# Kernel tuning notes

Measured on AMD Instinct MI355X. Metric: run time of the kernel, lower is better.

Reference implementation:

```python
import jax, jax.numpy as jnp
import numpy as np
from jax import lax
from jax.scipy.linalg import solve_triangular

T, DX, DZ = 8192, 1024, 16
POS_CONST = 1e-6
THRESH = 1e-5


def setup_inputs() -> dict:
    key = jax.random.key(0)
    ks = jax.random.split(key, 7)
    s = 0.02  # small init scale so A ~ I and AA is well-conditioned for Cholesky
    return {
        "X": jax.random.normal(ks[0], (T, DX), jnp.float32),
        "W1": jax.random.normal(ks[1], (DX, DX), jnp.float32) * s,
        "b1": jnp.zeros((DX,), jnp.float32),
        "Wmu": jax.random.normal(ks[2], (DX, DZ), jnp.float32) * s,
        "bmu": jnp.zeros((DZ,), jnp.float32),
        "WA": jax.random.normal(ks[3], (DX, DZ * DZ), jnp.float32) * s,
        "bA": jnp.zeros((DZ * DZ,), jnp.float32),
        "WB": jax.random.normal(ks[4], (2 * DX, DZ * DZ), jnp.float32) * s,
        "bB": jnp.zeros((DZ * DZ,), jnp.float32),
        "eps": jax.random.normal(ks[5], (T, DZ), jnp.float32),
    }


def _blk_tridag_chol(AA, BB):
    # AA: (T, d, d) diagonal blocks, BB: (T-1, d, d) lower off-diagonal blocks.
    # Returns lower-bidiagonal block Cholesky: chol_A (T,d,d), chol_B (T-1,d,d).
    L0 = jnp.linalg.cholesky(AA[0])

    def step(Lprev, ins):
        Bt, At = ins
        # C = Bt @ inv(Lprev)^T, via triangular solve: Lprev C^T = Bt^T
        C = solve_triangular(Lprev, Bt.T, lower=True).T
        Lt = jnp.linalg.cholesky(At - C @ C.T)
        return Lt, (Lt, C)

    _, (Ls, Cs) = lax.scan(step, L0, (BB, AA[1:]))
    return jnp.concatenate([L0[None], Ls]), Cs


def _blk_chol_inv_identity(chol_A, chol_B):
    # Forward substitution L x = b with b = block-diagonal identity blocks.
    I = jnp.eye(DZ, dtype=chol_A.dtype)
    x0 = solve_triangular(chol_A[0], I, lower=True)

    def step(xprev, ins):
        Lt, Ct = ins
        xt = solve_triangular(Lt, I - Ct @ xprev, lower=True)
        return xt, xt

    _, xs = lax.scan(step, x0, (chol_A[1:], chol_B))
    return jnp.concatenate([x0[None], xs])


def reference(X, W1, b1, Wmu, bmu, WA, bA, WB, bB, eps):
    # encode
    h = jax.nn.relu(X @ W1 + b1)                       # (T, dx)
    mu = h @ Wmu + bmu                                 # (T, dz)
    A = (h @ WA + bA).reshape(T, DZ, DZ) + jnp.eye(DZ, dtype=X.dtype)
    hcat = jnp.concatenate([h[1:], h[:-1]], axis=1)    # (T-1, 2*dx)
    B = (hcat @ WB + bB).reshape(T - 1, DZ, DZ)

    # make_psd
    diag_sq = jnp.einsum('tij,tkj->tik', A, A)         # A A^T
    offd_sq = jnp.einsum('tij,tkj->tik', B, B)         # B B^T
    offd_sq = jnp.concatenate([jnp.zeros((1, DZ, DZ), X.dtype), offd_sq])
    AA = diag_sq + offd_sq + POS_CONST * jnp.eye(DZ, dtype=X.dtype)
    BB = jnp.einsum('tij,tkj->tik', B, A[:-1])         # B A[:-1]^T

    chol_A, chol_B = _blk_tridag_chol(AA, BB)
    r = _blk_chol_inv_identity(chol_A, chol_B)         # (T, dz, dz)

    # relu(r - thresh) + thresh == max(r, thresh)
    r = jax.nn.relu(r - THRESH) + THRESH
    logdet = -jnp.log(jnp.einsum('tii->ti', r)).sum()
    entropy = logdet + DX * T / 2.0 * (1.0 + np.log(2.0 * np.pi))

    # sample_z = mu + r^T eps per block
    sample_z = mu + jnp.einsum('tji,tj->ti', r, eps)
    return entropy, sample_z
```

## Files before the change

### kernel.cpp

```cpp
#include <hip/hip_runtime.h>
#include <math.h>


#define T_STEPS 8192
#define DXX 1024

typedef __bf16 bf16x8 __attribute__((ext_vector_type(8)));
typedef float f32x4 __attribute__((ext_vector_type(4)));
typedef unsigned short u16x8 __attribute__((ext_vector_type(8)));
typedef unsigned short u16x4 __attribute__((ext_vector_type(4)));

typedef __attribute__((address_space(1))) unsigned int as1_uint;
typedef __attribute__((address_space(3))) unsigned int as3_uint;

#define DOT4(r, b) ((r).x*(b).x + (r).y*(b).y + (r).z*(b).z + (r).w*(b).w)

__device__ __forceinline__ unsigned short f2bf(float v) {
  unsigned int u = __float_as_uint(v);
  unsigned int r = (u + 0x7FFFu + ((u >> 16) & 1u)) >> 16;
  return (unsigned short)r;
}
__device__ __forceinline__ float bf2f(unsigned short b) {
  return __uint_as_float(((unsigned int)b) << 16);
}

__device__ __forceinline__ void gload16(const unsigned short* g, unsigned short* s) {
  __builtin_amdgcn_global_load_lds((as1_uint*)g, (as3_uint*)s, 16, 0, 0);
}

__global__ __launch_bounds__(256) void to_bf16(
    const float* __restrict__ src, unsigned short* __restrict__ dst, int n4)
{
  int idx = blockIdx.x * 256 + threadIdx.x;
  if (idx >= n4) return;
  float4 v = ((const float4*)src)[idx];
  u16x4 h;
  h[0] = f2bf(v.x); h[1] = f2bf(v.y); h[2] = f2bf(v.z); h[3] = f2bf(v.w);
  *(u16x4*)(dst + (size_t)idx * 4) = h;
}

__global__ __launch_bounds__(256) void transpose_bf16(
    const float* __restrict__ W, unsigned short* __restrict__ Tt, int K, int N)
{
  __shared__ float tile[32][33];
  int k0 = blockIdx.x * 32, n0 = blockIdx.y * 32;
  int c = threadIdx.x & 31, r = threadIdx.x >> 5;
#pragma unroll
  for (int e = 0; e < 4; ++e)
    tile[r + 8 * e][c] = W[(size_t)(k0 + r + 8 * e) * N + n0 + c];
  __syncthreads();
#pragma unroll
  for (int e = 0; e < 4; ++e)
    Tt[(size_t)(n0 + r + 8 * e) * K + k0 + c] = f2bf(tile[c][r + 8 * e]);
}

#define GBK 64

__global__ __launch_bounds__(256) void gemm_mfma(
    const unsigned short* __restrict__ Abf, const unsigned short* __restrict__ Bbf,
    const float* __restrict__ bias, int biasN, float* __restrict__ outF,
    unsigned short* __restrict__ outBf, int M, int N, int K, int mode)
{
  __shared__ __align__(16) unsigned short At[128 * GBK];
  __shared__ __align__(16) unsigned short Bt[128 * GBK];
  int tid = threadIdx.x;
  int l = tid & 63;
  int w = tid >> 6;
  int wm = w >> 1, wn = w & 1;
  int lane15 = l & 15, quad = l >> 4;
  int bm = blockIdx.y * 128, bn = blockIdx.x * 128;

  int srow = (w << 3) + (l >> 3);
  int jswz = (l & 7) ^ (srow & 7);
  const unsigned short* aSrc = Abf + (size_t)(bm + srow) * K + jswz * 8;
  const unsigned short* bSrc = Bbf + (size_t)(bn + srow) * K + jswz * 8;

  f32x4 acc[4][4];
#pragma unroll
  for (int mi = 0; mi < 4; ++mi)
#pragma unroll
    for (int ni = 0; ni < 4; ++ni) acc[mi][ni] = (f32x4){0.f, 0.f, 0.f, 0.f};

  for (int k0 = 0; k0 < K; k0 += GBK) {
#pragma unroll
    for (int i = 0; i < 4; ++i) {
      gload16(aSrc + (size_t)(i * 32) * K + k0, &At[(i * 32 + (w << 3)) * GBK]);
      gload16(bSrc + (size_t)(i * 32) * K + k0, &Bt[(i * 32 + (w << 3)) * GBK]);
    }
    __syncthreads();
#pragma unroll
    for (int h = 0; h < 2; ++h) {
      bf16x8 af[4], bfr[4];
#pragma unroll
      for (int mi = 0; mi < 4; ++mi) {
        int r = wm * 64 + mi * 16 + lane15;
        af[mi] = *(const bf16x8*)&At[r * GBK + ((((h << 2) + quad) ^ (lane15 & 7)) << 3)];
      }
#pragma unroll
      for (int ni = 0; ni < 4; ++ni) {
        int r = wn * 64 + ni * 16 + lane15;
        bfr[ni] = *(const bf16x8*)&Bt[r * GBK + ((((h << 2) + quad) ^ (lane15 & 7)) << 3)];
      }
#pragma unroll
      for (int mi = 0; mi < 4; ++mi)
#pragma unroll
        for (int ni = 0; ni < 4; ++ni)
          acc[mi][ni] = __builtin_amdgcn_mfma_f32_16x16x32_bf16(af[mi], bfr[ni], acc[mi][ni], 0, 0, 0);
    }
    __syncthreads();
  }

#pragma unroll
  for (int mi = 0; mi < 4; ++mi) {
#pragma unroll
    for (int ni = 0; ni < 4; ++ni) {
      int gc = bn + wn * 64 + ni * 16 + lane15;
      float bv = (bias && gc < biasN) ? bias[gc] : 0.f;
#pragma unroll
      for (int r = 0; r < 4; ++r) {
        int gr = bm + wm * 64 + mi * 16 + quad * 4 + r;
        float v = acc[mi][ni][r] + bv;
        if (mode == 1) {
          outBf[(size_t)gr * N + gc] = f2bf(fmaxf(v, 0.f));
        } else {
          outF[(size_t)gr * N + gc] = v;
        }
      }
    }
  }
}

__global__ __launch_bounds__(256) void mu_gemm(
    const unsigned short* __restrict__ hbf, const float* __restrict__ Wmu,
    const float* __restrict__ bmu, float* __restrict__ mu)
{
  int idx = blockIdx.x * 256 + threadIdx.x;
  int t = idx >> 4, j = idx & 15;
  const u16x8* ph = (const u16x8*)(hbf + (size_t)t * 1024);
  float s = bmu[j];
#pragma unroll 2
  for (int k8 = 0; k8 < 128; ++k8) {
    u16x8 hv = ph[k8];
#pragma unroll
    for (int e = 0; e < 8; ++e)
      s = fmaf(bf2f(hv[e]), Wmu[(k8 * 8 + e) * 16 + j], s);
  }
  mu[idx] = s;
}

__global__ __launch_bounds__(256) void make_psd(
    const float* __restrict__ Ccat, const float* __restrict__ bB,
    float* __restrict__ AAT, float* __restrict__ BBm, float* __restrict__ logdet)
{
  int t = blockIdx.x;
  int tid = threadIdx.x;
  int i = tid >> 4, j = tid & 15;
  if (t == 0 && tid == 0) *logdet = 0.f;
  __shared__ float a[16][17], bp[16][17], bq[16][17];
  a[i][j] = Ccat[(size_t)t * 768 + tid] + (i == j ? 1.f : 0.f);
  bp[i][j] = (t >= 1) ? (Ccat[(size_t)t * 768 + 256 + tid] + Ccat[(size_t)(t - 1) * 768 + 512 + tid] + bB[tid]) : 0.f;
  bool has_b = (t < T_STEPS - 1);
  if (has_b) bq[i][j] = Ccat[(size_t)(t + 1) * 768 + 256 + tid] + Ccat[(size_t)t * 768 + 512 + tid] + bB[tid];
  __syncthreads();
  float s = (i == j) ? 1e-6f : 0.f;
#pragma unroll
  for (int k = 0; k < 16; ++k) s += a[i][k] * a[j][k] + bp[i][k] * bp[j][k];
  AAT[(size_t)t * 256 + ((i >> 2) * 64 + j * 4 + (i & 3))] = s;
  if (has_b) {
    float s2 = 0.f;
#pragma unroll
    for (int k = 0; k < 16; ++k) s2 += bq[i][k] * a[j][k];
    BBm[(size_t)t * 256 + tid] = s2;
  }
}

#define RIC_S 8
#define RIC_W 16
#define RIC_NCH (T_STEPS / RIC_S)

__global__ __launch_bounds__(64) void riccati_wave(
    const float* __restrict__ AAT, const float* __restrict__ BBm,
    float* __restrict__ D)
{
  int l = threadIdx.x;
  int q = l >> 4, c = l & 15;
  int p = blockIdx.x;
  int t0 = p * RIC_S;
  int tw = t0 - RIC_W; if (tw < 0) tw = 0;
  int tend = t0 + RIC_S - 1;
  int row = l >> 2, cb = (l & 3) * 4;

  __shared__ float bbs[320], dis[320], ys[320];

  float4 a4 = *(const float4*)(AAT + (size_t)tw * 256 + l * 4);
  float dr[4] = {a4.x, a4.y, a4.z, a4.w};

  for (int t = tw; ; ++t) {
    if (t >= t0) {
#pragma unroll
      for (int u = 0; u < 4; ++u)
        D[(size_t)t * 256 + (q * 4 + u) * 16 + c] = dr[u];
    }
    if (t == tend) break;
    float4 bb4 = *(const float4*)(BBm + (size_t)t * 256 + l * 4);
    float4 aar = *(const float4*)(AAT + (size_t)(t + 1) * 256 + l * 4);

#pragma unroll
    for (int k = 0; k < 16; ++k) {
      const int kq = k >> 2, ku = k & 3;
      float rowv = __shfl(dr[ku], (kq << 4) | c);
      float pv   = __uint_as_float(__builtin_amdgcn_readlane(__float_as_uint(dr[ku]), (kq << 4) | k));
      float cv0  = __shfl(dr[0], (l & 48) | k);
      float cv1  = __shfl(dr[1], (l & 48) | k);
      float cv2  = __shfl(dr[2], (l & 48) | k);
      float cv3  = __shfl(dr[3], (l & 48) | k);
      float rpv  = __builtin_amdgcn_rcpf(pv);
      float t1v  = rowv * rpv;
      float cva[4] = {cv0, cv1, cv2, cv3};
#pragma unroll
      for (int u = 0; u < 4; ++u) {
        bool irow = (q == kq) && (u == ku);
        float nv = irow ? ((c == k) ? rpv : t1v)
                        : ((c == k) ? (-cva[u] * rpv) : fmaf(-cva[u], t1v, dr[u]));
        dr[u] = nv;
      }
    }

    *(float4*)&bbs[row * 20 + cb] = bb4;
#pragma unroll
    for (int u = 0; u < 4; ++u) dis[(q * 4 + u) * 20 + c] = dr[u];

    float y0a = 0, y1a = 0, y2a = 0, y3a = 0;
    float y0b = 0, y1b = 0, y2b = 0, y3b = 0;
#pragma unroll
    for (int kb = 0; kb < 4; ++kb) {
      float4 bc4 = *(const float4*)&bbs[c * 20 + kb * 4];
      float4 r0 = *(const float4*)&dis[(q * 4 + 0) * 20 + kb * 4];
      float4 r1 = *(const float4*)&dis[(q * 4 + 1) * 20 + kb * 4];
      float4 r2 = *(const float4*)&dis[(q * 4 + 2) * 20 + kb * 4];
      float4 r3 = *(const float4*)&dis[(q * 4 + 3) * 20 + kb * 4];
      if (kb & 1) {
        y0b += DOT4(r0, bc4); y1b += DOT4(r1, bc4); y2b += DOT4(r2, bc4); y3b += DOT4(r3, bc4);
      } else {
        y0a += DOT4(r0, bc4); y1a += DOT4(r1, bc4); y2a += DOT4(r2, bc4); y3a += DOT4(r3, bc4);
      }
    }
    ys[(q * 4 + 0) * 20 + c] = y0a + y0b;
    ys[(q * 4 + 1) * 20 + c] = y1a + y1b;
    ys[(q * 4 + 2) * 20 + c] = y2a + y2b;
    ys[(q * 4 + 3) * 20 + c] = y3a + y3b;

    float s0a = aar.x, s1a = aar.y, s2a = aar.z, s3a = aar.w;
    float s0b = 0, s1b = 0, s2b = 0, s3b = 0;
#pragma unroll
    for (int kb = 0; kb < 4; ++kb) {
      float4 b0 = *(const float4*)&bbs[(q * 4 + 0) * 20 + kb * 4];
      float4 b1 = *(const float4*)&bbs[(q * 4 + 1) * 20 + kb * 4];
      float4 b2 = *(const float4*)&bbs[(q * 4 + 2) * 20 + kb * 4];
      float4 b3 = *(const float4*)&bbs[(q * 4 + 3) * 20 + kb * 4];
      float yk0 = ys[(kb * 4 + 0) * 20 + c];
      float yk1 = ys[(kb * 4 + 1) * 20 + c];
      float yk2 = ys[(kb * 4 + 2) * 20 + c];
      float yk3 = ys[(kb * 4 + 3) * 20 + c];
      if (kb & 1) {
        s0b -= b0.x * yk0 + b0.y * yk1 + b0.z * yk2 + b0.w * yk3;
        s1b -= b1.x * yk0 + b1.y * yk1 + b1.z * yk2 + b1.w * yk3;
        s2b -= b2.x * yk0 + b2.y * yk1 + b2.z * yk2 + b2.w * yk3;
        s3b -= b3.x * yk0 + b3.y * yk1 + b3.z * yk2 + b3.w * yk3;
      } else {
        s0a -= b0.x * yk0 + b0.y * yk1 + b0.z * yk2 + b0.w * yk3;
        s1a -= b1.x * yk0 + b1.y * yk1 + b1.z * yk2 + b1.w * yk3;
        s2a -= b2.x * yk0 + b2.y * yk1 + b2.z * yk2 + b2.w * yk3;
        s3a -= b3.x * yk0 + b3.y * yk1 + b3.z * yk2 + b3.w * yk3;
      }
    }
    dr[0] = s0a + s0b; dr[1] = s1a + s1b; dr[2] = s2a + s2b; dr[3] = s3a + s3b;
  }
}

__global__ __launch_bounds__(256) void chol_inv(
    const float* __restrict__ D, const float* __restrict__ BBm,
    float* __restrict__ Linv, float* __restrict__ Cmat)
{
  int t = blockIdx.x;
  int tid = threadIdx.x;
  int i = tid >> 4, j = tid & 15;
  __shared__ float d[16][17], li[16][17], rhs[16][17], bb[16][17];
  d[i][j] = D[(size_t)t * 256 + tid];
  bool has_b = (t < T_STEPS - 1);
  if (has_b) bb[i][j] = BBm[(size_t)t * 256 + tid];
  rhs[i][j] = (i == j) ? 1.f : 0.f;
  __syncthreads();
  for (int k = 0; k < 16; ++k) {
    if (tid == k * 16 + k) d[k][k] = sqrtf(d[k][k]);
    __syncthreads();
    if (j == k && i > k) d[i][k] /= d[k][k];
    __syncthreads();
    if (i > k && j > k && j <= i) d[i][j] -= d[i][k] * d[j][k];
    __syncthreads();
  }
  for (int k = 0; k < 16; ++k) {
    if (i == k) li[k][j] = rhs[k][j] / d[k][k];
    __syncthreads();
    if (i > k) rhs[i][j] -= d[i][k] * li[k][j];
    __syncthreads();
  }
  Linv[(size_t)t * 256 + tid] = li[i][j];
  if (has_b) {
    float s = 0.f;
#pragma unroll
    for (int k = 0; k < 16; ++k) s += bb[i][k] * li[j][k];
    Cmat[(size_t)t * 256 + tid] = s;
  }
}

__global__ __launch_bounds__(256) void gmat_kernel(
    const float* __restrict__ Linv, const float* __restrict__ Cmat,
    float* __restrict__ Gmat)
{
  int t = blockIdx.x;
  int tid = threadIdx.x;
  int i = tid >> 4, j = tid & 15;
  if (t == 0) { Gmat[tid] = 0.f; return; }
  __shared__ float li[16][17], cm[16][17];
  li[i][j] = Linv[(size_t)t * 256 + tid];
  cm[i][j] = Cmat[(size_t)(t - 1) * 256 + tid];
  __syncthreads();
  float s = 0.f;
#pragma unroll
  for (int k = 0; k < 16; ++k) s -= li[i][k] * cm[k][j];
  Gmat[(size_t)t * 256 + tid] = s;
}

#define XS 8
#define XW 32
#define XNCH (T_STEPS / XS)

__global__ __launch_bounds__(64) void xseq_g(
    const float* __restrict__ Linv, const float* __restrict__ Gmat,
    const float* __restrict__ mu, const float* __restrict__ eps,
    float* __restrict__ out, float* __restrict__ logdet)
{
  int l = threadIdx.x;
  int q = l >> 4, c = l & 15;
  int p = blockIdx.x;
  int t0 = p * XS;
  int ts = t0 - XW; if (ts < 0) ts = 0;
  int row = l >> 2, cb = (l & 3) * 4;
  __shared__ float gs[320];
  float xr[4] = {0.f, 0.f, 0.f, 0.f};
  float logacc = 0.f;

  float4 g4 = *(const float4*)(Gmat + (size_t)ts * 256 + l * 4);
  float li[4];
#pragma unroll
  for (int u = 0; u < 4; ++u)
    li[u] = Linv[(size_t)ts * 256 + (q * 4 + u) * 16 + c];

  for (int t = ts; t < t0 + XS; ++t) {
    float4 g4n = {0.f, 0.f, 0.f, 0.f};
    float lin[4] = {0.f, 0.f, 0.f, 0.f};
    if (t + 1 < t0 + XS) {
      g4n = *(const float4*)(Gmat + (size_t)(t + 1) * 256 + l * 4);
#pragma unroll
      for (int u = 0; u < 4; ++u)
        lin[u] = Linv[(size_t)(t + 1) * 256 + (q * 4 + u) * 16 + c];
    }
    *(float4*)&gs[row * 20 + cb] = g4;

    float x0a = li[0], x1a = li[1], x2a = li[2], x3a = li[3];
    float x0b = 0.f, x1b = 0.f, x2b = 0.f, x3b = 0.f;
#pragma unroll
    for (int kb = 0; kb < 4; ++kb) {
      float4 r0 = *(const float4*)&gs[(q * 4 + 0) * 20 + kb * 4];
      float4 r1 = *(const float4*)&gs[(q * 4 + 1) * 20 + kb * 4];
      float4 r2 = *(const float4*)&gs[(q * 4 + 2) * 20 + kb * 4];
      float4 r3 = *(const float4*)&gs[(q * 4 + 3) * 20 + kb * 4];
      float a0[4] = {r0.x, r0.y, r0.z, r0.w};
      float a1[4] = {r1.x, r1.y, r1.z, r1.w};
      float a2[4] = {r2.x, r2.y, r2.z, r2.w};
      float a3[4] = {r3.x, r3.y, r3.z, r3.w};
#pragma unroll
      for (int e = 0; e < 4; ++e) {
        float xk = __shfl(xr[e], (kb << 4) | c);
        if (kb & 1) {
          x0b = fmaf(a0[e], xk, x0b);
          x1b = fmaf(a1[e], xk, x1b);
          x2b = fmaf(a2[e], xk, x2b);
          x3b = fmaf(a3[e], xk, x3b);
        } else {
          x0a = fmaf(a0[e], xk, x0a);
          x1a = fmaf(a1[e], xk, x1a);
          x2a = fmaf(a2[e], xk, x2a);
          x3a = fmaf(a3[e], xk, x3a);
        }
      }
    }
    float x0 = x0a + x0b, x1 = x1a + x1b, x2 = x2a + x2b, x3 = x3a + x3b;
    xr[0] = x0; xr[1] = x1; xr[2] = x2; xr[3] = x3;

    if (t >= t0) {
      float r0v = fmaxf(x0, 1e-5f), r1v = fmaxf(x1, 1e-5f);
      float r2v = fmaxf(x2, 1e-5f), r3v = fmaxf(x3, 1e-5f);
      if (q == (c >> 2)) {
        int sel = c & 3;
        float dv = sel == 0 ? r0v : (sel == 1 ? r1v : (sel == 2 ? r2v : r3v));
        logacc -= logf(dv);
      }
      float e0 = eps[(size_t)t * 16 + q * 4 + 0];
      float e1 = eps[(size_t)t * 16 + q * 4 + 1];
      float e2 = eps[(size_t)t * 16 + q * 4 + 2];
      float e3 = eps[(size_t)t * 16 + q * 4 + 3];
      float part = r0v * e0 + r1v * e1 + r2v * e2 + r3v * e3;
      part += __shfl_xor(part, 16);
      part += __shfl_xor(part, 32);
      if (q == 0) out[1 + (size_t)t * 16 + c] = mu[(size_t)t * 16 + c] + part;
    }
    g4 = g4n;
    li[0] = lin[0]; li[1] = lin[1]; li[2] = lin[2]; li[3] = lin[3];
  }
#pragma unroll
  for (int off = 1; off < 64; off <<= 1) logacc += __shfl_xor(logacc, off);
  if (l == 0) atomicAdd(logdet, logacc);
}

__global__ void finalize_entropy(const float* __restrict__ logdet, float* __restrict__ out)
{
  if (threadIdx.x == 0 && blockIdx.x == 0) {
    const double ENT = 0.5 * 1024.0 * 8192.0 * (1.0 + 1.8378770664093454);
    out[0] = (float)(ENT + (double)(*logdet));
  }
}

extern "C" void kernel_launch(void* const* d_in, const int* in_sizes, int n_in,
                              void* d_out, int out_size, void* d_ws, size_t ws_size,
                              hipStream_t stream)
{
  const float* X   = (const float*)d_in[0];
  const float* W1  = (const float*)d_in[1];
  const float* b1  = (const float*)d_in[2];
  const float* Wmu = (const float*)d_in[3];
  const float* bmu = (const float*)d_in[4];
  const float* WA  = (const float*)d_in[5];
  const float* bA  = (const float*)d_in[6];
  const float* WB  = (const float*)d_in[7];
  const float* bB  = (const float*)d_in[8];
  const float* eps = (const float*)d_in[9];
  float* out = (float*)d_out;
  char* ws  = (char*)d_ws;

  unsigned short* Xbf  = (unsigned short*)(ws + 0);
  unsigned short* W1t  = (unsigned short*)(ws + 16777216);
  unsigned short* hbf  = (unsigned short*)(ws + 25165824);
  unsigned short* Wcat = (unsigned short*)(ws + 50856960);
  float* Ccat   = (float*)(ws + 0);
  float* Cmat   = (float*)(ws + 0);
  float* AAT    = (float*)(ws + 25165824);
  float* Linv   = (float*)(ws + 25165824);
  float* BBp    = (float*)(ws + 33554432);
  float* Dws    = (float*)(ws + 41943040);
  float* Gmat   = (float*)(ws + 41943040);
  float* muw    = (float*)(ws + 50331648);
  float* logdet = (float*)(ws + 50855936);

  dim3 blk(256);

  to_bf16<<<dim3(8192), blk, 0, stream>>>(X, Xbf, 8192 * 1024 / 4);
  transpose_bf16<<<dim3(32, 32), blk, 0, stream>>>(W1, W1t, 1024, 1024);
  transpose_bf16<<<dim3(32, 8), blk, 0, stream>>>(WA, Wcat, 1024, 256);
  transpose_bf16<<<dim3(32, 8), blk, 0, stream>>>(WB, Wcat + 256 * 1024, 1024, 256);
  transpose_bf16<<<dim3(32, 8), blk, 0, stream>>>(WB + 1024 * 256, Wcat + 512 * 1024, 1024, 256);
  gemm_mfma<<<dim3(8, 64), blk, 0, stream>>>(Xbf, W1t, b1, 1024, nullptr, hbf, 8192, 1024, 1024, 1);
  gemm_mfma<<<dim3(6, 64), blk, 0, stream>>>(hbf, Wcat, bA, 256, Ccat, nullptr, 8192, 768, 1024, 0);
  mu_gemm<<<dim3(512), blk, 0, stream>>>(hbf, Wmu, bmu, muw);
  make_psd<<<dim3(T_STEPS), blk, 0, stream>>>(Ccat, bB, AAT, BBp, logdet);
  riccati_wave<<<dim3(RIC_NCH), dim3(64), 0, stream>>>(AAT, BBp, Dws);
  chol_inv<<<dim3(T_STEPS), blk, 0, stream>>>(Dws, BBp, Linv, Cmat);
  gmat_kernel<<<dim3(T_STEPS), blk, 0, stream>>>(Linv, Cmat, Gmat);
  xseq_g<<<dim3(XNCH), dim3(64), 0, stream>>>(Linv, Gmat, muw, eps, out, logdet);
  finalize_entropy<<<dim3(1), dim3(64), 0, stream>>>(logdet, out);
}
```

Before: 364.7 us.

## Fuse prep kernels, shorten warmup windows, and streamline per-block Cholesky inverse

The bf16 conversion of X and the four weight transposes are merged into a single launch, removing four kernel launches and their gaps. The warmup windows of the chunked Riccati and forward-substitution scans shrink (16→12 and 32→24 steps), cutting redundant recomputation. This relies on the recursions converging fast enough, so it risks accuracy. chol_inv now uses a reciprocal square root computed by every thread, keeps the RHS in registers, and needs fewer barriers per step.

Result: faster. 332.5 us (-8.8%).

```diff
diff --git a/kernel.cpp b/kernel.cpp
--- a/kernel.cpp
+++ b/kernel.cpp
@@ -28,30 +28,42 @@
   __builtin_amdgcn_global_load_lds((as1_uint*)g, (as3_uint*)s, 16, 0, 0);
 }
 
-__global__ __launch_bounds__(256) void to_bf16(
-    const float* __restrict__ src, unsigned short* __restrict__ dst, int n4)
-{
-  int idx = blockIdx.x * 256 + threadIdx.x;
-  if (idx >= n4) return;
-  float4 v = ((const float4*)src)[idx];
-  u16x4 h;
-  h[0] = f2bf(v.x); h[1] = f2bf(v.y); h[2] = f2bf(v.z); h[3] = f2bf(v.w);
-  *(u16x4*)(dst + (size_t)idx * 4) = h;
-}
-
-__global__ __launch_bounds__(256) void transpose_bf16(
-    const float* __restrict__ W, unsigned short* __restrict__ Tt, int K, int N)
-{
+__global__ __launch_bounds__(256) void prep(
+    const float* __restrict__ X, unsigned short* __restrict__ Xbf,
+    const float* __restrict__ W1, unsigned short* __restrict__ W1t,
+    const float* __restrict__ WA, const float* __restrict__ WB,
+    unsigned short* __restrict__ Wcat)
+{
+  int b = blockIdx.x;
+  if (b < 8192) {
+    int idx = b * 256 + threadIdx.x;
+    float4 v = ((const float4*)X)[idx];
+    u16x4 h;
+    h[0] = f2bf(v.x); h[1] = f2bf(v.y); h[2] = f2bf(v.z); h[3] = f2bf(v.w);
+    *(u16x4*)(Xbf + (size_t)idx * 4) = h;
+    return;
+  }
   __shared__ float tile[32][33];
-  int k0 = blockIdx.x * 32, n0 = blockIdx.y * 32;
-  int c = threadIdx.x & 31, r = threadIdx.x >> 5;
+  const float* W; unsigned short* Tt; int N, k0, n0;
+  int b2 = b - 8192;
+  if (b2 < 1024) {
+    W = W1; Tt = W1t; N = 1024;
+    k0 = (b2 & 31) * 32; n0 = (b2 >> 5) * 32;
+  } else {
+    int b3 = b2 - 1024;
+    int sel = b3 >> 8; int r = b3 & 255;
+    k0 = (r & 31) * 32; n0 = (r >> 5) * 32; N = 256;
+    W = (sel == 0) ? WA : (sel == 1 ? WB : WB + 1024 * 256);
+    Tt = Wcat + (size_t)sel * 256 * 1024;
+  }
+  int c = threadIdx.x & 31, rr = threadIdx.x >> 5;
 #pragma unroll
   for (int e = 0; e < 4; ++e)
-    tile[r + 8 * e][c] = W[(size_t)(k0 + r + 8 * e) * N + n0 + c];
+    tile[rr + 8 * e][c] = W[(size_t)(k0 + rr + 8 * e) * N + n0 + c];
   __syncthreads();
 #pragma unroll
   for (int e = 0; e < 4; ++e)
-    Tt[(size_t)(n0 + r + 8 * e) * K + k0 + c] = f2bf(tile[c][r + 8 * e]);
+    Tt[(size_t)(n0 + rr + 8 * e) * 1024 + k0 + c] = f2bf(tile[c][rr + 8 * e]);
 }
 
 #define GBK 64
@@ -175,7 +187,7 @@
 }
 
 #define RIC_S 8
-#define RIC_W 16
+#define RIC_W 12
 #define RIC_NCH (T_STEPS / RIC_S)
 
 __global__ __launch_bounds__(64) void riccati_wave(
@@ -285,25 +297,27 @@
   int t = blockIdx.x;
   int tid = threadIdx.x;
   int i = tid >> 4, j = tid & 15;
-  __shared__ float d[16][17], li[16][17], rhs[16][17], bb[16][17];
+  __shared__ float d[16][17], li[16][17], bb[16][17];
   d[i][j] = D[(size_t)t * 256 + tid];
   bool has_b = (t < T_STEPS - 1);
   if (has_b) bb[i][j] = BBm[(size_t)t * 256 + tid];
-  rhs[i][j] = (i == j) ? 1.f : 0.f;
-  __syncthreads();
+  float rsk[16];
+  float rhsv = (i == j) ? 1.f : 0.f;
+#pragma unroll
   for (int k = 0; k < 16; ++k) {
-    if (tid == k * 16 + k) d[k][k] = sqrtf(d[k][k]);
     __syncthreads();
-    if (j == k && i > k) d[i][k] /= d[k][k];
+    float dkk = d[k][k];
+    float rs = 1.0f / sqrtf(dkk);
+    rsk[k] = rs;
+    if (j == k && i > k) d[i][k] *= rs;
     __syncthreads();
     if (i > k && j > k && j <= i) d[i][j] -= d[i][k] * d[j][k];
+  }
+#pragma unroll
+  for (int k = 0; k < 16; ++k) {
+    if (i == k) li[k][j] = rhsv * rsk[k];
     __syncthreads();
-  }
-  for (int k = 0; k < 16; ++k) {
-    if (i == k) li[k][j] = rhs[k][j] / d[k][k];
-    __syncthreads();
-    if (i > k) rhs[i][j] -= d[i][k] * li[k][j];
-    __syncthreads();
+    if (i > k) rhsv -= d[i][k] * li[k][j];
   }
   Linv[(size_t)t * 256 + tid] = li[i][j];
   if (has_b) {
@@ -333,7 +347,7 @@
 }
 
 #define XS 8
-#define XW 32
+#define XW 24
 #define XNCH (T_STEPS / XS)
 
 __global__ __launch_bounds__(64) void xseq_g(
@@ -465,11 +479,7 @@
 
   dim3 blk(256);
 
-  to_bf16<<<dim3(8192), blk, 0, stream>>>(X, Xbf, 8192 * 1024 / 4);
-  transpose_bf16<<<dim3(32, 32), blk, 0, stream>>>(W1, W1t, 1024, 1024);
-  transpose_bf16<<<dim3(32, 8), blk, 0, stream>>>(WA, Wcat, 1024, 256);
-  transpose_bf16<<<dim3(32, 8), blk, 0, stream>>>(WB, Wcat + 256 * 1024, 1024, 256);
-  transpose_bf16<<<dim3(32, 8), blk, 0, stream>>>(WB + 1024 * 256, Wcat + 512 * 1024, 1024, 256);
+  prep<<<dim3(9984), blk, 0, stream>>>(X, Xbf, W1, W1t, WA, WB, Wcat);
   gemm_mfma<<<dim3(8, 64), blk, 0, stream>>>(Xbf, W1t, b1, 1024, nullptr, hbf, 8192, 1024, 1024, 1);
   gemm_mfma<<<dim3(6, 64), blk, 0, stream>>>(hbf, Wcat, bA, 256, Ccat, nullptr, 8192, 768, 1024, 0);
   mu_gemm<<<dim3(512), blk, 0, stream>>>(hbf, Wmu, bmu, muw);
```
